# Kernel optimization log

Hardware: AMD Instinct MI355X
Metric: run time of the kernel (lower is better)

Reference implementation:

```python
import jax, jax.numpy as jnp
import numpy as np

N, P, E = 100000, 10000, 500000
DN, DP, DK, SKIP, MLP_H = 256, 128, 100, 27, 64
E_MEAN, E_STD = 4.0, 2.0
ETA_MEAN, ETA_STD = 0.0, 1.5
ATT_NORM = 0.1  # 1/sqrt(100)
LN_EPS, RMS_EPS = 1e-5, 1e-6


def setup_inputs() -> dict:
    key = jax.random.key(0)
    ks = jax.random.split(key, 32)
    DIN = DN + SKIP  # 283
    s = 0.05
    inp = {
        'node_hidden': jax.random.normal(ks[0], (N, DN), jnp.float32),
        'energy': jax.random.uniform(ks[1], (N,), jnp.float32, 0.01, 1.0),
        'eta': jax.random.normal(ks[2], (N,), jnp.float32),
        'phi': jax.random.normal(ks[3], (N,), jnp.float32),
        'layer': jax.random.uniform(ks[4], (N,), jnp.float32),
        'eta_l': jax.random.normal(ks[5], (N, 6), jnp.float32),
        'phi_l': jax.random.normal(ks[6], (N, 6), jnp.float32),
        'ene_l': jax.random.normal(ks[7], (N, 6), jnp.float32),
        'track_feats': jax.random.uniform(ks[8], (N, 5), jnp.float32),
        'particle_hidden': jax.random.normal(ks[9], (P, DP), jnp.float32),
        'global_rep': jax.random.normal(ks[10], (P, DN), jnp.float32),
        'edge_src': jax.random.randint(ks[11], (E,), 0, N, jnp.int32),
        'edge_dst': jax.random.randint(ks[12], (E,), 0, P, jnp.int32),
        # learned params
        'W_key': jax.random.normal(ks[13], (DIN, DK), jnp.float32) * s,
        'b_key': jnp.zeros((DK,), jnp.float32),
        'W_val': jax.random.normal(ks[14], (DIN, DP), jnp.float32) * s,
        'b_val': jnp.zeros((DP,), jnp.float32),
        'W_q': jax.random.normal(ks[15], (DP + DN, DK), jnp.float32) * s,
        'b_q': jnp.zeros((DK,), jnp.float32),
        'W_ih': jax.random.normal(ks[16], (DP, 3 * DP), jnp.float32) * s,
        'b_ih': jnp.zeros((3 * DP,), jnp.float32),
        'W_hh': jax.random.normal(ks[17], (DP, 3 * DP), jnp.float32) * s,
        'b_hh': jnp.zeros((3 * DP,), jnp.float32),
        'ln_g': jnp.ones((DP,), jnp.float32),
        'ln_b': jnp.zeros((DP,), jnp.float32),
        'W1': jax.random.normal(ks[18], (DP, MLP_H), jnp.float32) * s,
        'b1': jnp.zeros((MLP_H,), jnp.float32),
        'W2': jax.random.normal(ks[19], (MLP_H, DP), jnp.float32) * s,
        'b2': jnp.zeros((DP,), jnp.float32),
        'rms_w': jnp.ones((DP,), jnp.float32),
        'lin_w': jax.random.normal(ks[20], (1, DP), jnp.float32),
    }
    return inp


def _forward(node_hidden, energy, eta, phi, layer, eta_l, phi_l, ene_l, track_feats,
             particle_hidden, global_rep,
             W_key, b_key, W_val, b_val, W_q, b_q, W_ih, b_ih, W_hh, b_hh,
             ln_g, ln_b, W1, b1, W2, b2, rms_w, lin_w, edge_src, edge_dst):
    # --- build node inputs: hidden rep + 27 skip scalars (same order as torch cat) ---
    skip = jnp.concatenate([
        ((jnp.log(energy) - E_MEAN) / E_STD)[:, None],
        ((eta - ETA_MEAN) / ETA_STD)[:, None],
        phi[:, None], layer[:, None],
        (eta_l - ETA_MEAN) / ETA_STD,  # eta_l1..l6
        phi_l, ene_l,
        track_feats,  # isTrack, nTracks, tracks_pt, nTracks_4, tracks_pt_4
    ], axis=1)  # [N, 27]
    x = jnp.concatenate([node_hidden, skip], axis=1)  # [N, 283]
    keys = x @ W_key + b_key      # [N, 100]
    vals = x @ W_val + b_val      # [N, DP]
    q = jnp.concatenate([particle_hidden, global_rep], axis=1) @ W_q + b_q  # [P, 100]

    # --- per-edge attention (note: node_update consumes RAW relu attention) ---
    att = jax.nn.relu(jnp.sum(keys[edge_src] * q[edge_dst], axis=1) * ATT_NORM)  # [E]
    msg = att[:, None] * vals[edge_src]                                          # [E, DP]
    ws = jax.ops.segment_sum(msg, edge_dst, num_segments=P)                      # [P, DP]

    # --- node update: rmsnorm * sigmoid(eltwise) gating, GRU, LN, MLP residual ---
    rms = ws * jax.lax.rsqrt(jnp.mean(ws * ws, axis=-1, keepdims=True) + RMS_EPS) * rms_w
    gated = rms * jax.nn.sigmoid(ws * lin_w)

    h = particle_hidden
    gi = gated @ W_ih + b_ih
    gh = h @ W_hh + b_hh
    i_r, i_z, i_n = jnp.split(gi, 3, axis=1)
    h_r, h_z, h_n = jnp.split(gh, 3, axis=1)
    r = jax.nn.sigmoid(i_r + h_r)
    z = jax.nn.sigmoid(i_z + h_z)
    n = jnp.tanh(i_n + r * h_n)
    h_new = (1.0 - z) * n + z * h

    mu = jnp.mean(h_new, axis=-1, keepdims=True)
    var = jnp.mean((h_new - mu) ** 2, axis=-1, keepdims=True)
    ln = (h_new - mu) * jax.lax.rsqrt(var + LN_EPS) * ln_g + ln_b
    mlp = jax.nn.relu(ln @ W1 + b1) @ W2 + b2
    return h + mlp  # updated particle 'node hidden rep'


def reference(node_hidden, energy, eta, phi, layer, eta_l, phi_l, ene_l, track_feats,
              particle_hidden, global_rep, edge_src, edge_dst,
              W_key, b_key, W_val, b_val, W_q, b_q, W_ih, b_ih, W_hh, b_hh,
              ln_g, ln_b, W1, b1, W2, b2, rms_w, lin_w):
    return _forward(node_hidden, energy, eta, phi, layer, eta_l, phi_l, ene_l, track_feats,
                    particle_hidden, global_rep,
                    W_key, b_key, W_val, b_val, W_q, b_q, W_ih, b_ih, W_hh, b_hh,
                    ln_g, ln_b, W1, b1, W2, b2, rms_w, lin_w, edge_src, edge_dst)
```

## Files before the change

### kernel.cpp

```cpp
#include <hip/hip_runtime.h>
#include <hip/hip_bf16.h>
#include <math.h>

#define THREADS 256

typedef __bf16 bf16_t;
typedef __bf16 bf16x8 __attribute__((ext_vector_type(8)));
typedef float f32x4 __attribute__((ext_vector_type(4)));

__device__ __forceinline__ float sigmoidf_(float x) { return 1.f / (1.f + expf(-x)); }

__device__ __forceinline__ void gload_lds16(const void* g, void* l) {
    __builtin_amdgcn_global_load_lds((const __attribute__((address_space(1))) void*)g,
                                     (__attribute__((address_space(3))) void*)l, 16, 0, 0);
}

__device__ __forceinline__ bf16x8 cvt8(float4 a, float4 b) {
    bf16x8 v;
    v[0] = (bf16_t)a.x; v[1] = (bf16_t)a.y; v[2] = (bf16_t)a.z; v[3] = (bf16_t)a.w;
    v[4] = (bf16_t)b.x; v[5] = (bf16_t)b.y; v[6] = (bf16_t)b.z; v[7] = (bf16_t)b.w;
    return v;
}

__global__ void prep_kernel(const float* __restrict__ W_key, const float* __restrict__ W_val,
                            const float* __restrict__ W_q, const float* __restrict__ b_key,
                            const float* __restrict__ b_val, const float* __restrict__ b_q,
                            bf16_t* __restrict__ WbfT, bf16_t* __restrict__ WqT,
                            float* __restrict__ bpn, float* __restrict__ bpq)
{
    int i = blockIdx.x * THREADS + threadIdx.x;
    const int NW = 256 * 288, NQ = 128 * 384;
    if (i < NW) {
        int c = i / 288, k = i - c * 288;
        float v = 0.f;
        if (k < 283) {
            if (c < 100) v = W_key[k * 100 + c];
            else if (c >= 128 && c < 256) v = W_val[k * 128 + (c - 128)];
        }
        WbfT[i] = (bf16_t)v;
    } else if (i < NW + NQ) {
        int j = i - NW;
        int c = j / 384, k = j - c * 384;
        WqT[j] = (bf16_t)((c < 100) ? W_q[k * 100 + c] : 0.f);
    } else if (i < NW + NQ + 256) {
        int c = i - NW - NQ;
        bpn[c] = (c < 100) ? b_key[c] : ((c >= 128 && c < 256) ? b_val[c - 128] : 0.f);
    } else if (i < NW + NQ + 256 + 128) {
        int c = i - NW - NQ - 256;
        bpq[c] = (c < 100) ? b_q[c] : 0.f;
    }
}

__global__ void prep2_kernel(const float* __restrict__ W_ih, const float* __restrict__ W_hh,
                             const float* __restrict__ b_ih, const float* __restrict__ b_hh,
                             const float* __restrict__ W1, const float* __restrict__ b1,
                             const float* __restrict__ W2,
                             bf16_t* __restrict__ BTg, bf16_t* __restrict__ W1Tp,
                             bf16_t* __restrict__ W2Tp, float* __restrict__ bgru,
                             float* __restrict__ b1p,
                             int* __restrict__ cnt, int twoP,
                             bf16_t* __restrict__ AG, int padStart, int padElems)
{
    int i = blockIdx.x * THREADS + threadIdx.x;
    const int NG = 768 * 256, N1 = 128 * 128, N2 = 128 * 128;
    const int NB = NG + N1 + N2 + 768 + 128;
    if (i < NG) {
        int c = i >> 8, k = i & 255;
        float v = 0.f;
        if (c < 384) { if (k < 128) v = W_ih[k * 384 + c]; }
        else         { if (k >= 128) v = W_hh[(k - 128) * 384 + (c - 384)]; }
        BTg[i] = (bf16_t)v;
    } else if (i < NG + N1) {
        int j = i - NG; int c = j >> 7, k = j & 127;
        W1Tp[j] = (bf16_t)((c < 64) ? W1[k * 64 + c] : 0.f);
    } else if (i < NG + N1 + N2) {
        int j = i - NG - N1; int c = j >> 7, k = j & 127;
        W2Tp[j] = (bf16_t)((k < 64) ? W2[k * 128 + c] : 0.f);
    } else if (i < NG + N1 + N2 + 768) {
        int c = i - NG - N1 - N2;
        bgru[c] = (c < 384) ? b_ih[c] : b_hh[c - 384];
    } else if (i < NB) {
        int c = i - NG - N1 - N2 - 768;
        b1p[c] = (c < 64) ? b1[c] : 0.f;
    } else if (i < NB + twoP) {
        cnt[i - NB] = 0;
    } else if (i < NB + twoP + padElems) {
        int j = i - NB - twoP;
        AG[(size_t)padStart * 256 + j] = (bf16_t)0.f;
    }
}

__global__ void skip_kernel(const float* __restrict__ energy, const float* __restrict__ eta,
                            const float* __restrict__ phi, const float* __restrict__ layer,
                            const float* __restrict__ eta_l, const float* __restrict__ phi_l,
                            const float* __restrict__ ene_l, const float* __restrict__ track,
                            bf16_t* __restrict__ skipb, int N_, int Mpad)
{
    int n = blockIdx.x * THREADS + threadIdx.x;
    if (n >= Mpad) return;
    float o[32];
#pragma unroll
    for (int j = 0; j < 32; ++j) o[j] = 0.f;
    if (n < N_) {
        o[0] = (logf(energy[n]) - 4.0f) * 0.5f;
        o[1] = eta[n] * (1.f / 1.5f);
        o[2] = phi[n];
        o[3] = layer[n];
#pragma unroll
        for (int j = 0; j < 6; ++j) o[4 + j]  = eta_l[n * 6 + j] * (1.f / 1.5f);
#pragma unroll
        for (int j = 0; j < 6; ++j) o[10 + j] = phi_l[n * 6 + j];
#pragma unroll
        for (int j = 0; j < 6; ++j) o[16 + j] = ene_l[n * 6 + j];
#pragma unroll
        for (int j = 0; j < 5; ++j) o[22 + j] = track[n * 5 + j];
    }
    bf16_t* dst = skipb + (size_t)n * 32;
#pragma unroll
    for (int g = 0; g < 4; ++g) {
        bf16x8 v;
#pragma unroll
        for (int j = 0; j < 8; ++j) v[j] = (bf16_t)o[g * 8 + j];
        *(bf16x8*)(dst + g * 8) = v;
    }
}

__global__ __launch_bounds__(256) void kv_gemm(
    const float* __restrict__ nh, const bf16_t* __restrict__ skipb,
    const bf16_t* __restrict__ BT, const float* __restrict__ bias,
    bf16_t* __restrict__ KVb, int N_)
{
    int tid = threadIdx.x;
    int w = tid >> 6, lane = tid & 63;
    int la = lane & 15, hi = lane >> 4;
    int row0 = blockIdx.x * 32;
    int col0 = w * 64;
    int r0 = row0 + la, r1 = row0 + 16 + la;
    bool ok0 = r0 < N_, ok1 = r1 < N_;
    const float* pa0 = nh + (size_t)r0 * 256 + hi * 8;
    const float* pa1 = nh + (size_t)r1 * 256 + hi * 8;

    f32x4 zero4 = {0.f, 0.f, 0.f, 0.f};
    f32x4 acc[2][4];
#pragma unroll
    for (int i = 0; i < 2; ++i)
#pragma unroll
        for (int j = 0; j < 4; ++j) acc[i][j] = zero4;

    for (int kt = 0; kt < 288; kt += 32) {
        bf16x8 a0, a1;
        if (kt < 256) {
            bf16x8 z = {};
            a0 = ok0 ? cvt8(*(const float4*)(pa0 + kt), *(const float4*)(pa0 + kt + 4)) : z;
            a1 = ok1 ? cvt8(*(const float4*)(pa1 + kt), *(const float4*)(pa1 + kt + 4)) : z;
        } else {
            a0 = *(const bf16x8*)(skipb + (size_t)r0 * 32 + hi * 8);
            a1 = *(const bf16x8*)(skipb + (size_t)r1 * 32 + hi * 8);
        }
        bf16x8 b[4];
#pragma unroll
        for (int j = 0; j < 4; ++j)
            b[j] = *(const bf16x8*)(BT + (size_t)(col0 + j * 16 + la) * 288 + kt + hi * 8);
#pragma unroll
        for (int j = 0; j < 4; ++j) {
            acc[0][j] = __builtin_amdgcn_mfma_f32_16x16x32_bf16(a0, b[j], acc[0][j], 0, 0, 0);
            acc[1][j] = __builtin_amdgcn_mfma_f32_16x16x32_bf16(a1, b[j], acc[1][j], 0, 0, 0);
        }
    }

#pragma unroll
    for (int j = 0; j < 4; ++j) {
        int col = col0 + j * 16 + la;
        float bb = bias[col];
#pragma unroll
        for (int i = 0; i < 2; ++i) {
#pragma unroll
            for (int r = 0; r < 4; ++r) {
                int row = row0 + i * 16 + hi * 4 + r;
                KVb[(size_t)row * 256 + col] = (bf16_t)(acc[i][j][r] + bb);
            }
        }
    }
}

template <int MODE>
__global__ __launch_bounds__(256) void mfma_gemm(
    const void* __restrict__ A0, const void* __restrict__ A1,
    const bf16_t* __restrict__ BT, const float* __restrict__ bias,
    void* __restrict__ out0v, const float* __restrict__ resid,
    int K, int Mlimit, int Nrows)
{
    __shared__ short AsS[64 * 32];
    __shared__ short BsS[128 * 32];
    int tid = threadIdx.x;
    int lane = tid & 63, w = tid >> 6;
    int la = lane & 15, hi = lane >> 4;
    int m0 = (w & 1) * 32, n0 = (w >> 1) * 64;
    int row0 = blockIdx.y * 64, col0 = blockIdx.x * 128;

    f32x4 zero4 = {0.f, 0.f, 0.f, 0.f};
    f32x4 acc[2][4];
#pragma unroll
    for (int i = 0; i < 2; ++i)
#pragma unroll
        for (int j = 0; j < 4; ++j) acc[i][j] = zero4;

    const int ra = tid >> 2, ka = (tid & 3) * 8;
    const int c1 = tid + 256;
    const int rb0 = tid >> 2, kb0 = (tid & 3) * 8;
    const int rb1 = c1 >> 2,  kb1 = (c1 & 3) * 8;

    for (int kt = 0; kt < K; kt += 32) {
        int gmA = row0 + ra;
        if (MODE == 1) {
            int gk = kt + ka;
            bf16x8 v = {};
            if (gmA < Nrows) {
                const float* s = (gk < 128) ? ((const float*)A0 + (size_t)gmA * 128 + gk)
                                            : ((const float*)A1 + (size_t)gmA * 256 + (gk - 128));
                v = cvt8(*(const float4*)s, *(const float4*)(s + 4));
            }
            *(bf16x8*)(AsS + (size_t)tid * 8) = v;
        } else {
            gload_lds16((const bf16_t*)A0 + (size_t)gmA * K + kt + ka,
                        AsS + (size_t)tid * 8);
        }
        gload_lds16(BT + (size_t)(col0 + rb0) * K + kt + kb0, BsS + (size_t)tid * 8);
        gload_lds16(BT + (size_t)(col0 + rb1) * K + kt + kb1, BsS + (size_t)c1 * 8);
        __syncthreads();
        bf16x8 a[2], b[4];
#pragma unroll
        for (int i = 0; i < 2; ++i)
            a[i] = *(const bf16x8*)(AsS + (m0 + i * 16 + la) * 32 + hi * 8);
#pragma unroll
        for (int j = 0; j < 4; ++j)
            b[j] = *(const bf16x8*)(BsS + (n0 + j * 16 + la) * 32 + hi * 8);
#pragma unroll
        for (int i = 0; i < 2; ++i)
#pragma unroll
            for (int j = 0; j < 4; ++j)
                acc[i][j] = __builtin_amdgcn_mfma_f32_16x16x32_bf16(a[i], b[j], acc[i][j], 0, 0, 0);
        __syncthreads();
    }

#pragma unroll
    for (int i = 0; i < 2; ++i) {
#pragma unroll
        for (int j = 0; j < 4; ++j) {
            int col = col0 + n0 + j * 16 + la;
            float bb = bias[col];
#pragma unroll
            for (int r = 0; r < 4; ++r) {
                int row = row0 + m0 + i * 16 + hi * 4 + r;
                float v = acc[i][j][r] + bb;
                if (MODE == 1) {
                    ((bf16_t*)out0v)[(size_t)row * 128 + col] = (bf16_t)v;
                } else if (MODE == 2) {
                    ((float*)out0v)[(size_t)row * 768 + col] = v;
                } else if (MODE == 3) {
                    ((bf16_t*)out0v)[(size_t)row * 128 + col] = (bf16_t)fmaxf(v, 0.f);
                } else {
                    if (row < Mlimit)
                        ((float*)out0v)[(size_t)row * 128 + col] = v + resid[(size_t)row * 128 + col];
                }
            }
        }
    }
}

__global__ void hist_kernel(const int* __restrict__ dst, int* __restrict__ cnt, int E_)
{
    int i = blockIdx.x * THREADS + threadIdx.x;
    if (i < E_) atomicAdd(&cnt[dst[i]], 1);
}

__global__ void scan_kernel(const int* __restrict__ cnt, int* __restrict__ offb, int P_)
{
    __shared__ int wsum[16];
    int tid = threadIdx.x;
    int lane = tid & 63, w = tid >> 6;
    int base = tid * 10;
    int c[10];
    int s = 0;
#pragma unroll
    for (int j = 0; j < 10; ++j) {
        int i = base + j;
        c[j] = (i < P_) ? cnt[i] : 0;
        s += c[j];
    }
    int pre = s;
    for (int o = 1; o < 64; o <<= 1) {
        int t = __shfl_up(pre, o);
        if (lane >= o) pre += t;
    }
    if (lane == 63) wsum[w] = pre;
    __syncthreads();
    if (w == 0 && lane < 16) {
        int v = wsum[lane];
        for (int o = 1; o < 16; o <<= 1) {
            int t = __shfl_up(v, o, 16);
            if (lane >= o) v += t;
        }
        wsum[lane] = v;
    }
    __syncthreads();
    int waveoff = (w == 0) ? 0 : wsum[w - 1];
    int run = waveoff + pre - s;
#pragma unroll
    for (int j = 0; j < 10; ++j) {
        int i = base + j;
        if (i <= P_) offb[i] = run;
        run += c[j];
    }
}

__global__ void fill_src_kernel(const int* __restrict__ dst, const int* __restrict__ src,
                                const int* __restrict__ offb, int* __restrict__ cur,
                                int* __restrict__ csrc, int E_)
{
    int i = blockIdx.x * THREADS + threadIdx.x;
    if (i < E_) {
        int d = dst[i];
        int pos = atomicAdd(&cur[d], 1);
        csrc[offb[d] + pos] = src[i];
    }
}

__global__ __launch_bounds__(256) void edge_kernel(
    const int* __restrict__ offb, const int* __restrict__ csrc,
    const bf16_t* __restrict__ KVb, const bf16_t* __restrict__ Qb,
    const float* __restrict__ ph, const float* __restrict__ rms_w,
    const float* __restrict__ lin_w, bf16_t* __restrict__ AG, int P_)
{
    int tid = threadIdx.x;
    int p = blockIdx.x * 4 + (tid >> 6);
    if (p >= P_) return;
    int lane = tid & 63;
    int c = lane & 15, g = lane >> 4;

    bf16x8 q8 = *(const bf16x8*)(Qb + (size_t)p * 128 + c * 8);
    float qf[8];
#pragma unroll
    for (int j = 0; j < 8; ++j) qf[j] = (float)q8[j];

    int s0 = offb[p], e0 = offb[p + 1];
    float acc[8] = {};

    int i = s0 + g;
    for (; i + 12 < e0; i += 16) {
        int n0 = csrc[i], n1 = csrc[i + 4], n2 = csrc[i + 8], n3 = csrc[i + 12];
        const bf16_t* b0 = KVb + (size_t)n0 * 256 + c * 8;
        const bf16_t* b1 = KVb + (size_t)n1 * 256 + c * 8;
        const bf16_t* b2 = KVb + (size_t)n2 * 256 + c * 8;
        const bf16_t* b3 = KVb + (size_t)n3 * 256 + c * 8;
        bf16x8 k0 = *(const bf16x8*)b0, v0 = *(const bf16x8*)(b0 + 128);
        bf16x8 k1 = *(const bf16x8*)b1, v1 = *(const bf16x8*)(b1 + 128);
        bf16x8 k2 = *(const bf16x8*)b2, v2 = *(const bf16x8*)(b2 + 128);
        bf16x8 k3 = *(const bf16x8*)b3, v3 = *(const bf16x8*)(b3 + 128);
        float d0 = 0.f, d1 = 0.f, d2 = 0.f, d3 = 0.f;
#pragma unroll
        for (int j = 0; j < 8; ++j) {
            d0 += qf[j] * (float)k0[j]; d1 += qf[j] * (float)k1[j];
            d2 += qf[j] * (float)k2[j]; d3 += qf[j] * (float)k3[j];
        }
        d0 += __shfl_xor(d0, 1); d1 += __shfl_xor(d1, 1); d2 += __shfl_xor(d2, 1); d3 += __shfl_xor(d3, 1);
        d0 += __shfl_xor(d0, 2); d1 += __shfl_xor(d1, 2); d2 += __shfl_xor(d2, 2); d3 += __shfl_xor(d3, 2);
        d0 += __shfl_xor(d0, 4); d1 += __shfl_xor(d1, 4); d2 += __shfl_xor(d2, 4); d3 += __shfl_xor(d3, 4);
        d0 += __shfl_xor(d0, 8); d1 += __shfl_xor(d1, 8); d2 += __shfl_xor(d2, 8); d3 += __shfl_xor(d3, 8);
        float a0 = fmaxf(d0 * 0.1f, 0.f), a1 = fmaxf(d1 * 0.1f, 0.f);
        float a2 = fmaxf(d2 * 0.1f, 0.f), a3 = fmaxf(d3 * 0.1f, 0.f);
#pragma unroll
        for (int j = 0; j < 8; ++j)
            acc[j] += a0 * (float)v0[j] + a1 * (float)v1[j]
                    + a2 * (float)v2[j] + a3 * (float)v3[j];
    }
    for (; i < e0; i += 4) {
        int nA = csrc[i];
        const bf16_t* bA = KVb + (size_t)nA * 256 + c * 8;
        bf16x8 kA = *(const bf16x8*)bA;
        bf16x8 vA = *(const bf16x8*)(bA + 128);
        float dA = 0.f;
#pragma unroll
        for (int j = 0; j < 8; ++j) dA += qf[j] * (float)kA[j];
        dA += __shfl_xor(dA, 1);
        dA += __shfl_xor(dA, 2);
        dA += __shfl_xor(dA, 4);
        dA += __shfl_xor(dA, 8);
        float aA = fmaxf(dA * 0.1f, 0.f);
#pragma unroll
        for (int j = 0; j < 8; ++j) acc[j] += aA * (float)vA[j];
    }

#pragma unroll
    for (int j = 0; j < 8; ++j) {
        acc[j] += __shfl_xor(acc[j], 16);
        acc[j] += __shfl_xor(acc[j], 32);
    }

    float ss = 0.f;
#pragma unroll
    for (int j = 0; j < 8; ++j) ss += acc[j] * acc[j];
    ss += __shfl_xor(ss, 1); ss += __shfl_xor(ss, 2); ss += __shfl_xor(ss, 4); ss += __shfl_xor(ss, 8);
    float scale = rsqrtf(ss * (1.f / 128.f) + 1e-6f);
    if (g == 0) {
        int cb = c * 8;
        const float* hp = ph + (size_t)p * 128 + cb;
        float4 ha = *(const float4*)hp, hb = *(const float4*)(hp + 4);
        float hv[8] = {ha.x, ha.y, ha.z, ha.w, hb.x, hb.y, hb.z, hb.w};
        bf16x8 gv, hvb;
#pragma unroll
        for (int j = 0; j < 8; ++j) {
            float wsv = acc[j];
            float rv = wsv * scale * rms_w[cb + j];
            gv[j] = (bf16_t)(rv * sigmoidf_(wsv * lin_w[cb + j]));
            hvb[j] = (bf16_t)hv[j];
        }
        *(bf16x8*)(AG + (size_t)p * 256 + cb) = gv;
        *(bf16x8*)(AG + (size_t)p * 256 + 128 + cb) = hvb;
    }
}

__global__ void gru_ln_kernel(const float* __restrict__ G768, const float* __restrict__ ph,
                              const float* __restrict__ ln_g, const float* __restrict__ ln_b,
                              bf16_t* __restrict__ LNb, int P_, int Mq)
{
    int tid = threadIdx.x;
    int g = tid >> 4, s = tid & 15;
    int p = blockIdx.x * 16 + g;
    if (p >= Mq) return;
    int cb = s * 8;
    if (p >= P_) {
        bf16x8 z = {};
        *(bf16x8*)(LNb + (size_t)p * 128 + cb) = z;
        return;
    }
    const float* G = G768 + (size_t)p * 768;
    float ir[8], iz[8], in_[8], hr[8], hz[8], hn_[8], hv[8];
#pragma unroll
    for (int q = 0; q < 2; ++q) {
        float4 v;
        v = *(const float4*)(G + cb + q * 4);        ir[q*4]=v.x; ir[q*4+1]=v.y; ir[q*4+2]=v.z; ir[q*4+3]=v.w;
        v = *(const float4*)(G + 128 + cb + q * 4);  iz[q*4]=v.x; iz[q*4+1]=v.y; iz[q*4+2]=v.z; iz[q*4+3]=v.w;
        v = *(const float4*)(G + 256 + cb + q * 4);  in_[q*4]=v.x; in_[q*4+1]=v.y; in_[q*4+2]=v.z; in_[q*4+3]=v.w;
        v = *(const float4*)(G + 384 + cb + q * 4);  hr[q*4]=v.x; hr[q*4+1]=v.y; hr[q*4+2]=v.z; hr[q*4+3]=v.w;
        v = *(const float4*)(G + 512 + cb + q * 4);  hz[q*4]=v.x; hz[q*4+1]=v.y; hz[q*4+2]=v.z; hz[q*4+3]=v.w;
        v = *(const float4*)(G + 640 + cb + q * 4);  hn_[q*4]=v.x; hn_[q*4+1]=v.y; hn_[q*4+2]=v.z; hn_[q*4+3]=v.w;
        v = *(const float4*)(ph + (size_t)p * 128 + cb + q * 4);
        hv[q*4]=v.x; hv[q*4+1]=v.y; hv[q*4+2]=v.z; hv[q*4+3]=v.w;
    }
    float hn[8];
    float sm = 0.f, sq = 0.f;
#pragma unroll
    for (int j = 0; j < 8; ++j) {
        float r = sigmoidf_(ir[j] + hr[j]);
        float z = sigmoidf_(iz[j] + hz[j]);
        float n = tanhf(in_[j] + r * hn_[j]);
        hn[j] = (1.f - z) * n + z * hv[j];
        sm += hn[j]; sq += hn[j] * hn[j];
    }
    sm += __shfl_xor(sm, 1); sm += __shfl_xor(sm, 2); sm += __shfl_xor(sm, 4); sm += __shfl_xor(sm, 8);
    sq += __shfl_xor(sq, 1); sq += __shfl_xor(sq, 2); sq += __shfl_xor(sq, 4); sq += __shfl_xor(sq, 8);
    float mu = sm * (1.f / 128.f);
    float var = sq * (1.f / 128.f) - mu * mu;
    float iv = rsqrtf(var + 1e-5f);
    bf16x8 o;
#pragma unroll
    for (int j = 0; j < 8; ++j) {
        int c = cb + j;
        o[j] = (bf16_t)((hn[j] - mu) * iv * ln_g[c] + ln_b[c]);
    }
    *(bf16x8*)(LNb + (size_t)p * 128 + cb) = o;
}

extern "C" void kernel_launch(void* const* d_in, const int* in_sizes, int n_in,
                              void* d_out, int out_size, void* d_ws, size_t ws_size,
                              hipStream_t stream)
{
    const float* nh      = (const float*)d_in[0];
    const float* energy  = (const float*)d_in[1];
    const float* eta     = (const float*)d_in[2];
    const float* phi     = (const float*)d_in[3];
    const float* layer   = (const float*)d_in[4];
    const float* eta_l   = (const float*)d_in[5];
    const float* phi_l   = (const float*)d_in[6];
    const float* ene_l   = (const float*)d_in[7];
    const float* track   = (const float*)d_in[8];
    const float* ph      = (const float*)d_in[9];
    const float* grep    = (const float*)d_in[10];
    const int*   esrc    = (const int*)d_in[11];
    const int*   edst    = (const int*)d_in[12];
    const float* W_key   = (const float*)d_in[13];
    const float* b_key   = (const float*)d_in[14];
    const float* W_val   = (const float*)d_in[15];
    const float* b_val   = (const float*)d_in[16];
    const float* W_q     = (const float*)d_in[17];
    const float* b_q     = (const float*)d_in[18];
    const float* W_ih    = (const float*)d_in[19];
    const float* b_ih    = (const float*)d_in[20];
    const float* W_hh    = (const float*)d_in[21];
    const float* b_hh    = (const float*)d_in[22];
    const float* ln_g    = (const float*)d_in[23];
    const float* ln_b    = (const float*)d_in[24];
    const float* W1      = (const float*)d_in[25];
    const float* b1      = (const float*)d_in[26];
    const float* W2      = (const float*)d_in[27];
    const float* b2      = (const float*)d_in[28];
    const float* rms_w   = (const float*)d_in[29];
    const float* lin_w   = (const float*)d_in[30];

    const int N = in_sizes[1];
    const int P = in_sizes[9] / 128;
    const int E = in_sizes[11];
    const int Mpad = ((N + 127) / 128) * 128;
    const int Mq   = ((P + 127) / 128) * 128;

    char* base = (char*)d_ws;
    size_t off = 0;
    auto alloc = [&](size_t bytes) { void* p = base + off; off = (off + bytes + 255) & ~(size_t)255; return p; };
    bf16_t* skipb = (bf16_t*)alloc((size_t)Mpad * 32 * 2);
    bf16_t* WbfT  = (bf16_t*)alloc(256 * 288 * 2);
    bf16_t* WqT   = (bf16_t*)alloc(128 * 384 * 2);
    float*  bpn   = (float*)alloc(256 * 4);
    float*  bpq   = (float*)alloc(128 * 4);
    bf16_t* KVb   = (bf16_t*)alloc((size_t)Mpad * 256 * 2);
    bf16_t* Qb    = (bf16_t*)alloc((size_t)Mq * 128 * 2);
    int*    cnt   = (int*)alloc((size_t)(2 * P) * 4);
    int*    cur   = cnt + P;
    int*    offb  = (int*)alloc((size_t)(P + 1) * 4);
    int*    csrc  = (int*)alloc((size_t)E * 4);
    bf16_t* AG    = (bf16_t*)alloc((size_t)Mq * 256 * 2);
    bf16_t* BTg   = (bf16_t*)alloc(768 * 256 * 2);
    bf16_t* W1Tp  = (bf16_t*)alloc(128 * 128 * 2);
    bf16_t* W2Tp  = (bf16_t*)alloc(128 * 128 * 2);
    float*  bgru  = (float*)alloc(768 * 4);
    float*  b1p   = (float*)alloc(128 * 4);
    float*  G768  = (float*)alloc((size_t)Mq * 768 * 4);
    bf16_t* LNb   = (bf16_t*)alloc((size_t)Mq * 128 * 2);
    bf16_t* M1    = (bf16_t*)alloc((size_t)Mq * 128 * 2);

    {
        int total = 256 * 288 + 128 * 384 + 256 + 128;
        prep_kernel<<<(total + THREADS - 1) / THREADS, THREADS, 0, stream>>>(
            W_key, W_val, W_q, b_key, b_val, b_q, WbfT, WqT, bpn, bpq);
        int padElems = (Mq - P) * 256;
        int total2 = 768 * 256 + 128 * 128 + 128 * 128 + 768 + 128 + 2 * P + padElems;
        prep2_kernel<<<(total2 + THREADS - 1) / THREADS, THREADS, 0, stream>>>(
            W_ih, W_hh, b_ih, b_hh, W1, b1, W2, BTg, W1Tp, W2Tp, bgru, b1p,
            cnt, 2 * P, AG, P, padElems);
        skip_kernel<<<(Mpad + THREADS - 1) / THREADS, THREADS, 0, stream>>>(
            energy, eta, phi, layer, eta_l, phi_l, ene_l, track, skipb, N, Mpad);
    }
    kv_gemm<<<Mpad / 32, THREADS, 0, stream>>>(nh, skipb, WbfT, bpn, KVb, N);
    mfma_gemm<1><<<dim3(1, Mq / 64), THREADS, 0, stream>>>(
        ph, grep, WqT, bpq, Qb, nullptr, 384, 0, P);
    hist_kernel<<<(E + THREADS - 1) / THREADS, THREADS, 0, stream>>>(edst, cnt, E);
    scan_kernel<<<1, 1024, 0, stream>>>(cnt, offb, P);
    fill_src_kernel<<<(E + THREADS - 1) / THREADS, THREADS, 0, stream>>>(
        edst, esrc, offb, cur, csrc, E);
    edge_kernel<<<(P + 3) / 4, THREADS, 0, stream>>>(
        offb, csrc, KVb, Qb, ph, rms_w, lin_w, AG, P);
    mfma_gemm<2><<<dim3(6, Mq / 64), THREADS, 0, stream>>>(
        AG, nullptr, BTg, bgru, G768, nullptr, 256, 0, Mq);
    gru_ln_kernel<<<Mq / 16, THREADS, 0, stream>>>(G768, ph, ln_g, ln_b, LNb, P, Mq);
    mfma_gemm<3><<<dim3(1, Mq / 64), THREADS, 0, stream>>>(
        LNb, nullptr, W1Tp, b1p, M1, nullptr, 128, 0, Mq);
    mfma_gemm<4><<<dim3(1, Mq / 64), THREADS, 0, stream>>>(
        M1, nullptr, W2Tp, b2, d_out, ph, 128, P, Mq);
}
```

Measured before the change: 263.9 us.

## Merge prep kernels, split KV GEMM into single-wave LDS tiles, fuse MLP

Merges the two weight-prep kernels into one launch. The KV projection GEMM now runs as one 64-thread wave per block over a 2D grid, staging A and B tiles in LDS instead of each wave reading global memory directly. The two MFMA GEMMs for the MLP are replaced by one fp32 SIMT kernel that computes relu(LN·W1+b1)·W2+b2 plus the residual. This removes several launches and intermediate buffers, but the MLP loses its matrix-core path and the KV GEMM adds barriers per k-step.

```diff
diff --git a/kernel.cpp b/kernel.cpp
--- a/kernel.cpp
+++ b/kernel.cpp
@@ -22,70 +22,58 @@
     return v;
 }
 
-__global__ void prep_kernel(const float* __restrict__ W_key, const float* __restrict__ W_val,
-                            const float* __restrict__ W_q, const float* __restrict__ b_key,
-                            const float* __restrict__ b_val, const float* __restrict__ b_q,
-                            bf16_t* __restrict__ WbfT, bf16_t* __restrict__ WqT,
-                            float* __restrict__ bpn, float* __restrict__ bpq)
-{
-    int i = blockIdx.x * THREADS + threadIdx.x;
+__global__ void prep_all(const float* __restrict__ W_key, const float* __restrict__ W_val,
+                         const float* __restrict__ W_q, const float* __restrict__ b_key,
+                         const float* __restrict__ b_val, const float* __restrict__ b_q,
+                         bf16_t* __restrict__ WbfT, bf16_t* __restrict__ WqT,
+                         float* __restrict__ bpn, float* __restrict__ bpq,
+                         const float* __restrict__ W_ih, const float* __restrict__ W_hh,
+                         const float* __restrict__ b_ih, const float* __restrict__ b_hh,
+                         bf16_t* __restrict__ BTg, float* __restrict__ bgru,
+                         int* __restrict__ cnt, int twoP,
+                         bf16_t* __restrict__ AG, int padStart, int padElems)
+{
+    int i0 = blockIdx.x * THREADS + threadIdx.x;
     const int NW = 256 * 288, NQ = 128 * 384;
-    if (i < NW) {
-        int c = i / 288, k = i - c * 288;
-        float v = 0.f;
-        if (k < 283) {
-            if (c < 100) v = W_key[k * 100 + c];
-            else if (c >= 128 && c < 256) v = W_val[k * 128 + (c - 128)];
-        }
-        WbfT[i] = (bf16_t)v;
-    } else if (i < NW + NQ) {
-        int j = i - NW;
-        int c = j / 384, k = j - c * 384;
-        WqT[j] = (bf16_t)((c < 100) ? W_q[k * 100 + c] : 0.f);
-    } else if (i < NW + NQ + 256) {
-        int c = i - NW - NQ;
-        bpn[c] = (c < 100) ? b_key[c] : ((c >= 128 && c < 256) ? b_val[c - 128] : 0.f);
-    } else if (i < NW + NQ + 256 + 128) {
-        int c = i - NW - NQ - 256;
-        bpq[c] = (c < 100) ? b_q[c] : 0.f;
-    }
-}
-
-__global__ void prep2_kernel(const float* __restrict__ W_ih, const float* __restrict__ W_hh,
-                             const float* __restrict__ b_ih, const float* __restrict__ b_hh,
-                             const float* __restrict__ W1, const float* __restrict__ b1,
-                             const float* __restrict__ W2,
-                             bf16_t* __restrict__ BTg, bf16_t* __restrict__ W1Tp,
-                             bf16_t* __restrict__ W2Tp, float* __restrict__ bgru,
-                             float* __restrict__ b1p,
-                             int* __restrict__ cnt, int twoP,
-                             bf16_t* __restrict__ AG, int padStart, int padElems)
-{
-    int i = blockIdx.x * THREADS + threadIdx.x;
-    const int NG = 768 * 256, N1 = 128 * 128, N2 = 128 * 128;
-    const int NB = NG + N1 + N2 + 768 + 128;
+    const int T1 = NW + NQ + 256 + 128;
+    if (i0 < T1) {
+        int i = i0;
+        if (i < NW) {
+            int c = i / 288, k = i - c * 288;
+            float v = 0.f;
+            if (k < 283) {
+                if (c < 100) v = W_key[k * 100 + c];
+                else if (c >= 128 && c < 256) v = W_val[k * 128 + (c - 128)];
+            }
+            WbfT[i] = (bf16_t)v;
+        } else if (i < NW + NQ) {
+            int j = i - NW;
+            int c = j / 384, k = j - c * 384;
+            WqT[j] = (bf16_t)((c < 100) ? W_q[k * 100 + c] : 0.f);
+        } else if (i < NW + NQ + 256) {
+            int c = i - NW - NQ;
+            bpn[c] = (c < 100) ? b_key[c] : ((c >= 128 && c < 256) ? b_val[c - 128] : 0.f);
+        } else {
+            int c = i - NW - NQ - 256;
+            bpq[c] = (c < 100) ? b_q[c] : 0.f;
+        }
+        return;
+    }
+    int i = i0 - T1;
+    const int NG = 768 * 256;
     if (i < NG) {
         int c = i >> 8, k = i & 255;
         float v = 0.f;
         if (c < 384) { if (k < 128) v = W_ih[k * 384 + c]; }
         else         { if (k >= 128) v = W_hh[(k - 128) * 384 + (c - 384)]; }
         BTg[i] = (bf16_t)v;
-    } else if (i < NG + N1) {
-        int j = i - NG; int c = j >> 7, k = j & 127;
-        W1Tp[j] = (bf16_t)((c < 64) ? W1[k * 64 + c] : 0.f);
-    } else if (i < NG + N1 + N2) {
-        int j = i - NG - N1; int c = j >> 7, k = j & 127;
-        W2Tp[j] = (bf16_t)((k < 64) ? W2[k * 128 + c] : 0.f);
-    } else if (i < NG + N1 + N2 + 768) {
-        int c = i - NG - N1 - N2;
+    } else if (i < NG + 768) {
+        int c = i - NG;
         bgru[c] = (c < 384) ? b_ih[c] : b_hh[c - 384];
-    } else if (i < NB) {
-        int c = i - NG - N1 - N2 - 768;
-        b1p[c] = (c < 64) ? b1[c] : 0.f;
-    } else if (i < NB + twoP) {
-        cnt[i - NB] = 0;
-    } else if (i < NB + twoP + padElems) {
-        int j = i - NB - twoP;
+    } else if (i < NG + 768 + twoP) {
+        cnt[i - NG - 768] = 0;
+    } else if (i < NG + 768 + twoP + padElems) {
+        int j = i - NG - 768 - twoP;
         AG[(size_t)padStart * 256 + j] = (bf16_t)0.f;
     }
 }
@@ -125,21 +113,21 @@
     }
 }
 
-__global__ __launch_bounds__(256) void kv_gemm(
+__global__ __launch_bounds__(64) void kv_gemm1w(
     const float* __restrict__ nh, const bf16_t* __restrict__ skipb,
     const bf16_t* __restrict__ BT, const float* __restrict__ bias,
     bf16_t* __restrict__ KVb, int N_)
 {
-    int tid = threadIdx.x;
-    int w = tid >> 6, lane = tid & 63;
+    __shared__ short As[32 * 32];
+    __shared__ short Bs[64 * 32];
+    int lane = threadIdx.x;
     int la = lane & 15, hi = lane >> 4;
     int row0 = blockIdx.x * 32;
-    int col0 = w * 64;
-    int r0 = row0 + la, r1 = row0 + 16 + la;
-    bool ok0 = r0 < N_, ok1 = r1 < N_;
-    const float* pa0 = nh + (size_t)r0 * 256 + hi * 8;
-    const float* pa1 = nh + (size_t)r1 * 256 + hi * 8;
-
+    int col0 = blockIdx.y * 64;
+
+    const int ca0 = lane, ca1 = lane + 64;
+    const int ra0 = ca0 >> 2, ko0 = (ca0 & 3) * 8;
+    const int ra1 = ca1 >> 2, ko1 = (ca1 & 3) * 8;
     f32x4 zero4 = {0.f, 0.f, 0.f, 0.f};
     f32x4 acc[2][4];
 #pragma unroll
@@ -148,24 +136,43 @@
         for (int j = 0; j < 4; ++j) acc[i][j] = zero4;
 
     for (int kt = 0; kt < 288; kt += 32) {
-        bf16x8 a0, a1;
         if (kt < 256) {
-            bf16x8 z = {};
-            a0 = ok0 ? cvt8(*(const float4*)(pa0 + kt), *(const float4*)(pa0 + kt + 4)) : z;
-            a1 = ok1 ? cvt8(*(const float4*)(pa1 + kt), *(const float4*)(pa1 + kt + 4)) : z;
+            int g0 = row0 + ra0, g1 = row0 + ra1;
+            bf16x8 v0 = {}, v1 = {};
+            if (g0 < N_) {
+                const float* s = nh + (size_t)g0 * 256 + kt + ko0;
+                v0 = cvt8(*(const float4*)s, *(const float4*)(s + 4));
+            }
+            if (g1 < N_) {
+                const float* s = nh + (size_t)g1 * 256 + kt + ko1;
+                v1 = cvt8(*(const float4*)s, *(const float4*)(s + 4));
+            }
+            *(bf16x8*)(As + (size_t)ca0 * 8) = v0;
+            *(bf16x8*)(As + (size_t)ca1 * 8) = v1;
         } else {
-            a0 = *(const bf16x8*)(skipb + (size_t)r0 * 32 + hi * 8);
-            a1 = *(const bf16x8*)(skipb + (size_t)r1 * 32 + hi * 8);
-        }
-        bf16x8 b[4];
+            gload_lds16(skipb + (size_t)(row0 + ra0) * 32 + ko0, As + (size_t)ca0 * 8);
+            gload_lds16(skipb + (size_t)(row0 + ra1) * 32 + ko1, As + (size_t)ca1 * 8);
+        }
+#pragma unroll
+        for (int q = 0; q < 4; ++q) {
+            int c = lane + q * 64;
+            int rb = c >> 2, kb = (c & 3) * 8;
+            gload_lds16(BT + (size_t)(col0 + rb) * 288 + kt + kb, Bs + (size_t)c * 8);
+        }
+        __syncthreads();
+        bf16x8 a[2], b[4];
+#pragma unroll
+        for (int i = 0; i < 2; ++i)
+            a[i] = *(const bf16x8*)(As + (i * 16 + la) * 32 + hi * 8);
 #pragma unroll
         for (int j = 0; j < 4; ++j)
-            b[j] = *(const bf16x8*)(BT + (size_t)(col0 + j * 16 + la) * 288 + kt + hi * 8);
-#pragma unroll
-        for (int j = 0; j < 4; ++j) {
-            acc[0][j] = __builtin_amdgcn_mfma_f32_16x16x32_bf16(a0, b[j], acc[0][j], 0, 0, 0);
-            acc[1][j] = __builtin_amdgcn_mfma_f32_16x16x32_bf16(a1, b[j], acc[1][j], 0, 0, 0);
-        }
+            b[j] = *(const bf16x8*)(Bs + (j * 16 + la) * 32 + hi * 8);
+#pragma unroll
+        for (int i = 0; i < 2; ++i)
+#pragma unroll
+            for (int j = 0; j < 4; ++j)
+                acc[i][j] = __builtin_amdgcn_mfma_f32_16x16x32_bf16(a[i], b[j], acc[i][j], 0, 0, 0);
+        __syncthreads();
     }
 
 #pragma unroll
@@ -187,8 +194,7 @@
 __global__ __launch_bounds__(256) void mfma_gemm(
     const void* __restrict__ A0, const void* __restrict__ A1,
     const bf16_t* __restrict__ BT, const float* __restrict__ bias,
-    void* __restrict__ out0v, const float* __restrict__ resid,
-    int K, int Mlimit, int Nrows)
+    void* __restrict__ out0v, int K, int Nrows)
 {
     __shared__ short AsS[64 * 32];
     __shared__ short BsS[128 * 32];
@@ -253,16 +259,8 @@
             for (int r = 0; r < 4; ++r) {
                 int row = row0 + m0 + i * 16 + hi * 4 + r;
                 float v = acc[i][j][r] + bb;
-                if (MODE == 1) {
-                    ((bf16_t*)out0v)[(size_t)row * 128 + col] = (bf16_t)v;
-                } else if (MODE == 2) {
-                    ((float*)out0v)[(size_t)row * 768 + col] = v;
-                } else if (MODE == 3) {
-                    ((bf16_t*)out0v)[(size_t)row * 128 + col] = (bf16_t)fmaxf(v, 0.f);
-                } else {
-                    if (row < Mlimit)
-                        ((float*)out0v)[(size_t)row * 128 + col] = v + resid[(size_t)row * 128 + col];
-                }
+                if (MODE == 1) ((bf16_t*)out0v)[(size_t)row * 128 + col] = (bf16_t)v;
+                else           ((float*)out0v)[(size_t)row * 768 + col] = v;
             }
         }
     }
@@ -470,6 +468,55 @@
         o[j] = (bf16_t)((hn[j] - mu) * iv * ln_g[c] + ln_b[c]);
     }
     *(bf16x8*)(LNb + (size_t)p * 128 + cb) = o;
+}
+
+__global__ __launch_bounds__(256) void mlp_kernel(
+    const bf16_t* __restrict__ LNb, const float* __restrict__ ph,
+    const float* __restrict__ W1, const float* __restrict__ b1,
+    const float* __restrict__ W2, const float* __restrict__ b2,
+    float* __restrict__ out, int P_)
+{
+    __shared__ float lnl[16 * 132];
+    __shared__ float h1l[16 * 68];
+    int tid = threadIdx.x;
+    int g = tid >> 4, s = tid & 15;
+    int p0 = blockIdx.x * 16;
+    int p = p0 + g;
+
+    for (int i = tid; i < 16 * 128; i += 256) {
+        int row = i >> 7, c = i & 127;
+        lnl[row * 132 + c] = (float)LNb[(size_t)(p0 + row) * 128 + c];
+    }
+    __syncthreads();
+
+    int m0 = s * 4;
+    float am[4] = {b1[m0], b1[m0 + 1], b1[m0 + 2], b1[m0 + 3]};
+    for (int k = 0; k < 128; ++k) {
+        float lk = lnl[g * 132 + k];
+        float4 w = *(const float4*)(W1 + k * 64 + m0);
+        am[0] += lk * w.x; am[1] += lk * w.y; am[2] += lk * w.z; am[3] += lk * w.w;
+    }
+    h1l[g * 68 + m0 + 0] = fmaxf(am[0], 0.f);
+    h1l[g * 68 + m0 + 1] = fmaxf(am[1], 0.f);
+    h1l[g * 68 + m0 + 2] = fmaxf(am[2], 0.f);
+    h1l[g * 68 + m0 + 3] = fmaxf(am[3], 0.f);
+    __syncthreads();
+
+    if (p >= P_) return;
+    int cb = s * 8;
+    const float* hp = ph + (size_t)p * 128 + cb;
+    float4 ha = *(const float4*)hp, hb = *(const float4*)(hp + 4);
+    float o[8] = {ha.x + b2[cb], ha.y + b2[cb + 1], ha.z + b2[cb + 2], ha.w + b2[cb + 3],
+                  hb.x + b2[cb + 4], hb.y + b2[cb + 5], hb.z + b2[cb + 6], hb.w + b2[cb + 7]};
+    for (int m = 0; m < 64; ++m) {
+        float hm = h1l[g * 68 + m];
+        const float* wp = W2 + m * 128 + cb;
+        float4 wa = *(const float4*)wp, wb = *(const float4*)(wp + 4);
+        o[0] += hm * wa.x; o[1] += hm * wa.y; o[2] += hm * wa.z; o[3] += hm * wa.w;
+        o[4] += hm * wb.x; o[5] += hm * wb.y; o[6] += hm * wb.z; o[7] += hm * wb.w;
+    }
+    *(float4*)(out + (size_t)p * 128 + cb)     = make_float4(o[0], o[1], o[2], o[3]);
+    *(float4*)(out + (size_t)p * 128 + cb + 4) = make_float4(o[4], o[5], o[6], o[7]);
 }
 
 extern "C" void kernel_launch(void* const* d_in, const int* in_sizes, int n_in,
@@ -530,29 +577,23 @@
     int*    csrc  = (int*)alloc((size_t)E * 4);
     bf16_t* AG    = (bf16_t*)alloc((size_t)Mq * 256 * 2);
     bf16_t* BTg   = (bf16_t*)alloc(768 * 256 * 2);
-    bf16_t* W1Tp  = (bf16_t*)alloc(128 * 128 * 2);
-    bf16_t* W2Tp  = (bf16_t*)alloc(128 * 128 * 2);
     float*  bgru  = (float*)alloc(768 * 4);
-    float*  b1p   = (float*)alloc(128 * 4);
     float*  G768  = (float*)alloc((size_t)Mq * 768 * 4);
     bf16_t* LNb   = (bf16_t*)alloc((size_t)Mq * 128 * 2);
-    bf16_t* M1    = (bf16_t*)alloc((size_t)Mq * 128 * 2);
 
     {
-        int total = 256 * 288 + 128 * 384 + 256 + 128;
-        prep_kernel<<<(total + THREADS - 1) / THREADS, THREADS, 0, stream>>>(
-            W_key, W_val, W_q, b_key, b_val, b_q, WbfT, WqT, bpn, bpq);
         int padElems = (Mq - P) * 256;
-        int total2 = 768 * 256 + 128 * 128 + 128 * 128 + 768 + 128 + 2 * P + padElems;
-        prep2_kernel<<<(total2 + THREADS - 1) / THREADS, THREADS, 0, stream>>>(
-            W_ih, W_hh, b_ih, b_hh, W1, b1, W2, BTg, W1Tp, W2Tp, bgru, b1p,
-            cnt, 2 * P, AG, P, padElems);
+        int T1 = 256 * 288 + 128 * 384 + 256 + 128;
+        int T2 = 768 * 256 + 768 + 2 * P + padElems;
+        prep_all<<<(T1 + T2 + THREADS - 1) / THREADS, THREADS, 0, stream>>>(
+            W_key, W_val, W_q, b_key, b_val, b_q, WbfT, WqT, bpn, bpq,
+            W_ih, W_hh, b_ih, b_hh, BTg, bgru, cnt, 2 * P, AG, P, padElems);
         skip_kernel<<<(Mpad + THREADS - 1) / THREADS, THREADS, 0, stream>>>(
             energy, eta, phi, layer, eta_l, phi_l, ene_l, track, skipb, N, Mpad);
     }
-    kv_gemm<<<Mpad / 32, THREADS, 0, stream>>>(nh, skipb, WbfT, bpn, KVb, N);
+    kv_gemm1w<<<dim3(Mpad / 32, 4), 64, 0, stream>>>(nh, skipb, WbfT, bpn, KVb, N);
     mfma_gemm<1><<<dim3(1, Mq / 64), THREADS, 0, stream>>>(
-        ph, grep, WqT, bpq, Qb, nullptr, 384, 0, P);
+        ph, grep, WqT, bpq, Qb, 384, P);
     hist_kernel<<<(E + THREADS - 1) / THREADS, THREADS, 0, stream>>>(edst, cnt, E);
     scan_kernel<<<1, 1024, 0, stream>>>(cnt, offb, P);
     fill_src_kernel<<<(E + THREADS - 1) / THREADS, THREADS, 0, stream>>>(
@@ -560,10 +601,7 @@
     edge_kernel<<<(P + 3) / 4, THREADS, 0, stream>>>(
         offb, csrc, KVb, Qb, ph, rms_w, lin_w, AG, P);
     mfma_gemm<2><<<dim3(6, Mq / 64), THREADS, 0, stream>>>(
-        AG, nullptr, BTg, bgru, G768, nullptr, 256, 0, Mq);
+        AG, nullptr, BTg, bgru, G768, 256, Mq);
     gru_ln_kernel<<<Mq / 16, THREADS, 0, stream>>>(G768, ph, ln_g, ln_b, LNb, P, Mq);
-    mfma_gemm<3><<<dim3(1, Mq / 64), THREADS, 0, stream>>>(
-        LNb, nullptr, W1Tp, b1p, M1, nullptr, 128, 0, Mq);
-    mfma_gemm<4><<<dim3(1, Mq / 64), THREADS, 0, stream>>>(
-        M1, nullptr, W2Tp, b2, d_out, ph, 128, P, Mq);
-}
+    mlp_kernel<<<Mq / 16, THREADS, 0, stream>>>(LNb, ph, W1, b1, W2, b2, (float*)d_out, P);
+}
```

Result: no change. 261.1 us (-1.1%).
